# Optimization experiments

Hardware: AMD Instinct MI355X
Metric: run time of the kernel (lower is better)

Reference implementation:

```python
import jax, jax.numpy as jnp
import numpy as np

B, NELEC, NATOMS, SH_PER_ATOM, NORB, NCTR = 512, 100, 20, 30, 300, 2
NBAS = NATOMS * SH_PER_ATOM  # 600 == NORB * NCTR


def _ipow(x, k):
    # x**k for integer k in {0,1,2}; safe for negative x (cartesian harmonics)
    return jnp.where(k == 0, jnp.ones_like(x), jnp.where(k == 1, x, x * x))


def setup_inputs() -> dict:
    key = jax.random.key(0)
    ks = jax.random.split(key, 7)
    pos = jax.random.normal(ks[0], (B, NELEC * 3), jnp.float32)
    atom_coords = jax.random.normal(ks[1], (NATOMS, 3), jnp.float32)
    bas_exp = jax.random.uniform(ks[2], (NBAS,), jnp.float32, 0.5, 3.0)
    bas_n = jax.random.randint(ks[3], (NBAS,), 0, 3).astype(jnp.float32)
    norm_cst = jax.random.uniform(ks[4], (NBAS,), jnp.float32, 0.5, 1.5)
    bas_coeffs = jax.random.normal(ks[5], (NBAS,), jnp.float32)
    bas_kxyz = jax.random.randint(ks[6], (NBAS, 3), 0, 3)  # kx, ky, kz exponents
    index_ctr = jnp.repeat(jnp.arange(NORB, dtype=jnp.int32), NCTR)  # nbas -> norb
    return {"pos": pos, "atom_coords": atom_coords, "bas_exp": bas_exp,
            "bas_n": bas_n, "norm_cst": norm_cst, "bas_coeffs": bas_coeffs,
            "bas_kxyz": bas_kxyz, "index_ctr": index_ctr}


def reference(pos, atom_coords, bas_exp, bas_n, norm_cst, bas_coeffs, bas_kxyz, index_ctr):
    # gather: per-shell atom coordinates  (NBAS, 3)
    bas_coords = jnp.repeat(atom_coords, SH_PER_ATOM, axis=0)
    # electron - basis-center displacement  (B, Nelec, NBAS, 3)
    xyz = pos.reshape(-1, NELEC, 1, 3) - bas_coords[None, None]
    r2 = jnp.sum(xyz * xyz, axis=-1)                 # (B, Nelec, NBAS)
    r = jnp.sqrt(r2)
    # radial_gaussian: r^n * exp(-alpha r^2)
    R = jnp.power(r, bas_n) * jnp.exp(-bas_exp * r2)
    # cartesian harmonics: x^kx * y^ky * z^kz
    Y = (_ipow(xyz[..., 0], bas_kxyz[:, 0]) *
         _ipow(xyz[..., 1], bas_kxyz[:, 1]) *
         _ipow(xyz[..., 2], bas_kxyz[:, 2]))
    # ao kernel + contraction (segment-sum over basis fns into orbitals)
    vals = (norm_cst * bas_coeffs) * R * Y           # (B, Nelec, NBAS)
    ao = jnp.zeros((pos.shape[0], NELEC, NORB), vals.dtype).at[:, :, index_ctr].add(vals)
    return ao
```

## Files before the change

### kernel.cpp

```cpp
#include <hip/hip_runtime.h>

#define BATCH   512
#define NELEC   100
#define NATOMS  20
#define SH      30
#define NORB    300
#define NBAS    600
#define NROWS   (BATCH * NELEC)
#define ROWS    32
#define NBLOCKS (NROWS / ROWS)
#define BLOCK   320

#define LOG2E 1.4426950408889634f

__global__ __launch_bounds__(BLOCK, 8) void ao_kernel(
    const float* __restrict__ pos,
    const float* __restrict__ atom_coords,
    const float* __restrict__ bas_exp,
    const float* __restrict__ bas_n,
    const float* __restrict__ norm_cst,
    const float* __restrict__ bas_coeffs,
    const int*   __restrict__ bas_kxyz,
    float*       __restrict__ out)
{
    __shared__ float4 spos4[ROWS];

    const int t    = threadIdx.x;
    const int row0 = blockIdx.x * ROWS;

    if (t < ROWS * 3) {
        ((float*)spos4)[(t / 3) * 4 + (t % 3)] = pos[(size_t)row0 * 3 + t];
    }
    __syncthreads();

    if (t < NORB) {
        const int s0 = 2 * t, s1 = s0 + 1;

        const float al0 = bas_exp[s0] * LOG2E;
        const float al1 = bas_exp[s1] * LOG2E;
        const int   n0  = (int)bas_n[s0];
        const int   n1  = (int)bas_n[s1];
        const float c0  = norm_cst[s0] * bas_coeffs[s0];
        const float c1  = norm_cst[s1] * bas_coeffs[s1];
        const int  kx0 = bas_kxyz[3 * s0 + 0], ky0 = bas_kxyz[3 * s0 + 1], kz0 = bas_kxyz[3 * s0 + 2];
        const int  kx1 = bas_kxyz[3 * s1 + 0], ky1 = bas_kxyz[3 * s1 + 1], kz1 = bas_kxyz[3 * s1 + 2];
        const int  at  = s0 / SH;
        const float ax = atom_coords[3 * at + 0];
        const float ay = atom_coords[3 * at + 1];
        const float az = atom_coords[3 * at + 2];

        float* op = out + (size_t)row0 * NORB + t;

#pragma unroll 2
        for (int r = 0; r < ROWS; ++r) {
            const float4 p = spos4[r];

            const float dx = p.x - ax, dy = p.y - ay, dz = p.z - az;
            const float r2 = fmaf(dx, dx, fmaf(dy, dy, dz * dz));
            const float rr = sqrtf(r2);

            float e0 = exp2f(-al0 * r2);
            float R0 = (n0 == 0) ? 1.0f : ((n0 == 1) ? rr : r2);
            float yx = (kx0 == 0) ? 1.0f : dx;  yx = (kx0 == 2) ? yx * dx : yx;
            float yy = (ky0 == 0) ? 1.0f : dy;  yy = (ky0 == 2) ? yy * dy : yy;
            float yz = (kz0 == 0) ? 1.0f : dz;  yz = (kz0 == 2) ? yz * dz : yz;
            float v  = c0 * R0 * e0 * (yx * yy * yz);

            float e1 = exp2f(-al1 * r2);
            float R1 = (n1 == 0) ? 1.0f : ((n1 == 1) ? rr : r2);
            yx = (kx1 == 0) ? 1.0f : dx;  yx = (kx1 == 2) ? yx * dx : yx;
            yy = (ky1 == 0) ? 1.0f : dy;  yy = (ky1 == 2) ? yy * dy : yy;
            yz = (kz1 == 0) ? 1.0f : dz;  yz = (kz1 == 2) ? yz * dz : yz;
            v += c1 * R1 * e1 * (yx * yy * yz);

            *op = v;
            op += NORB;
        }
    }
}

extern "C" void kernel_launch(void* const* d_in, const int* in_sizes, int n_in,
                              void* d_out, int out_size, void* d_ws, size_t ws_size,
                              hipStream_t stream) {
    const float* pos         = (const float*)d_in[0];
    const float* atom_coords = (const float*)d_in[1];
    const float* bas_exp     = (const float*)d_in[2];
    const float* bas_n       = (const float*)d_in[3];
    const float* norm_cst    = (const float*)d_in[4];
    const float* bas_coeffs  = (const float*)d_in[5];
    const int*   bas_kxyz    = (const int*)d_in[6];
    float* out = (float*)d_out;

    ao_kernel<<<NBLOCKS, BLOCK, 0, stream>>>(pos, atom_coords, bas_exp, bas_n,
                                             norm_cst, bas_coeffs, bas_kxyz, out);
}
```

Measured before the change: 115.7 us.

## Vectorize basis-pair math with packed FMA and raw exp2/sqrt intrinsics

Replaces the per-basis selects with polynomial masks evaluated through packed two-wide FMAs, so both contracted basis functions are computed with packed-math instructions. It uses raw hardware exp2 and sqrt intrinsics, loads the per-thread parameters as vector loads before the barrier, and halves rows per block to launch more blocks. The raw intrinsics skip denormal and range handling, and smaller blocks repeat the parameter setup more often.

```diff
diff --git a/kernel.cpp b/kernel.cpp
--- a/kernel.cpp
+++ b/kernel.cpp
@@ -7,11 +7,16 @@
 #define NORB    300
 #define NBAS    600
 #define NROWS   (BATCH * NELEC)
-#define ROWS    32
-#define NBLOCKS (NROWS / ROWS)
+#define GROWS   16
+#define NBLOCKS (NROWS / GROWS)
 #define BLOCK   320
 
 #define LOG2E 1.4426950408889634f
+
+typedef float f2 __attribute__((ext_vector_type(2)));
+__device__ __forceinline__ f2 fma2(f2 a, f2 b, f2 c) {
+    return __builtin_elementwise_fma(a, b, c);
+}
 
 __global__ __launch_bounds__(BLOCK, 8) void ao_kernel(
     const float* __restrict__ pos,
@@ -23,57 +28,78 @@
     const int*   __restrict__ bas_kxyz,
     float*       __restrict__ out)
 {
-    __shared__ float4 spos4[ROWS];
+    __shared__ float4 spos4[GROWS];
 
     const int t    = threadIdx.x;
-    const int row0 = blockIdx.x * ROWS;
+    const int row0 = blockIdx.x * GROWS;
 
-    if (t < ROWS * 3) {
+    float2 ex2, nn2, nc2, bc2;
+    int2 k01, k23, k45;
+    float ax = 0.f, ay = 0.f, az = 0.f;
+    if (t < NORB) {
+        ex2 = ((const float2*)bas_exp)[t];
+        nn2 = ((const float2*)bas_n)[t];
+        nc2 = ((const float2*)norm_cst)[t];
+        bc2 = ((const float2*)bas_coeffs)[t];
+        k01 = ((const int2*)bas_kxyz)[3 * t + 0];
+        k23 = ((const int2*)bas_kxyz)[3 * t + 1];
+        k45 = ((const int2*)bas_kxyz)[3 * t + 2];
+        const int at = (2 * t) / SH;
+        ax = atom_coords[3 * at + 0];
+        ay = atom_coords[3 * at + 1];
+        az = atom_coords[3 * at + 2];
+    }
+
+    if (t < GROWS * 3) {
         ((float*)spos4)[(t / 3) * 4 + (t % 3)] = pos[(size_t)row0 * 3 + t];
     }
     __syncthreads();
 
     if (t < NORB) {
-        const int s0 = 2 * t, s1 = s0 + 1;
-
-        const float al0 = bas_exp[s0] * LOG2E;
-        const float al1 = bas_exp[s1] * LOG2E;
-        const int   n0  = (int)bas_n[s0];
-        const int   n1  = (int)bas_n[s1];
-        const float c0  = norm_cst[s0] * bas_coeffs[s0];
-        const float c1  = norm_cst[s1] * bas_coeffs[s1];
-        const int  kx0 = bas_kxyz[3 * s0 + 0], ky0 = bas_kxyz[3 * s0 + 1], kz0 = bas_kxyz[3 * s0 + 2];
-        const int  kx1 = bas_kxyz[3 * s1 + 0], ky1 = bas_kxyz[3 * s1 + 1], kz1 = bas_kxyz[3 * s1 + 2];
-        const int  at  = s0 / SH;
-        const float ax = atom_coords[3 * at + 0];
-        const float ay = atom_coords[3 * at + 1];
-        const float az = atom_coords[3 * at + 2];
+        const float c0 = nc2.x * bc2.x;
+        const float c1 = nc2.y * bc2.y;
+        const f2 al = { -ex2.x * LOG2E, -ex2.y * LOG2E };
+        const int n0 = (int)nn2.x, n1 = (int)nn2.y;
+        const f2 q0 = { (n0 == 0) ? c0 : 0.f, (n1 == 0) ? c1 : 0.f };
+        const f2 q1 = { (n0 == 1) ? c0 : 0.f, (n1 == 1) ? c1 : 0.f };
+        const f2 q2 = { (n0 == 2) ? c0 : 0.f, (n1 == 2) ? c1 : 0.f };
+        const int kx0 = k01.x, ky0 = k01.y, kz0 = k23.x;
+        const int kx1 = k23.y, ky1 = k45.x, kz1 = k45.y;
+        const f2 mx0 = { (float)(kx0 == 0), (float)(kx1 == 0) };
+        const f2 mx1 = { (float)(kx0 == 1), (float)(kx1 == 1) };
+        const f2 mx2 = { (float)(kx0 == 2), (float)(kx1 == 2) };
+        const f2 my0 = { (float)(ky0 == 0), (float)(ky1 == 0) };
+        const f2 my1 = { (float)(ky0 == 1), (float)(ky1 == 1) };
+        const f2 my2 = { (float)(ky0 == 2), (float)(ky1 == 2) };
+        const f2 mz0 = { (float)(kz0 == 0), (float)(kz1 == 0) };
+        const f2 mz1 = { (float)(kz0 == 1), (float)(kz1 == 1) };
+        const f2 mz2 = { (float)(kz0 == 2), (float)(kz1 == 2) };
 
         float* op = out + (size_t)row0 * NORB + t;
 
-#pragma unroll 2
-        for (int r = 0; r < ROWS; ++r) {
+#pragma unroll 4
+        for (int r = 0; r < GROWS; ++r) {
             const float4 p = spos4[r];
 
             const float dx = p.x - ax, dy = p.y - ay, dz = p.z - az;
-            const float r2 = fmaf(dx, dx, fmaf(dy, dy, dz * dz));
-            const float rr = sqrtf(r2);
+            const float r2s = fmaf(dx, dx, fmaf(dy, dy, dz * dz));
+            const float rr  = __builtin_amdgcn_sqrtf(r2s);
 
-            float e0 = exp2f(-al0 * r2);
-            float R0 = (n0 == 0) ? 1.0f : ((n0 == 1) ? rr : r2);
-            float yx = (kx0 == 0) ? 1.0f : dx;  yx = (kx0 == 2) ? yx * dx : yx;
-            float yy = (ky0 == 0) ? 1.0f : dy;  yy = (ky0 == 2) ? yy * dy : yy;
-            float yz = (kz0 == 0) ? 1.0f : dz;  yz = (kz0 == 2) ? yz * dz : yz;
-            float v  = c0 * R0 * e0 * (yx * yy * yz);
+            const f2 dxv = { dx, dx }, dyv = { dy, dy }, dzv = { dz, dz };
+            const f2 r2v = { r2s, r2s }, rrv = { rr, rr };
 
-            float e1 = exp2f(-al1 * r2);
-            float R1 = (n1 == 0) ? 1.0f : ((n1 == 1) ? rr : r2);
-            yx = (kx1 == 0) ? 1.0f : dx;  yx = (kx1 == 2) ? yx * dx : yx;
-            yy = (ky1 == 0) ? 1.0f : dy;  yy = (ky1 == 2) ? yy * dy : yy;
-            yz = (kz1 == 0) ? 1.0f : dz;  yz = (kz1 == 2) ? yz * dz : yz;
-            v += c1 * R1 * e1 * (yx * yy * yz);
+            const f2 ta = al * r2v;
+            f2 e;
+            e.x = __builtin_amdgcn_exp2f(ta.x);
+            e.y = __builtin_amdgcn_exp2f(ta.y);
 
-            *op = v;
+            const f2 cR = fma2(rrv, q1, fma2(r2v, q2, q0));
+            const f2 yx = fma2(dxv, fma2(dxv, mx2, mx1), mx0);
+            const f2 yy = fma2(dyv, fma2(dyv, my2, my1), my0);
+            const f2 yz = fma2(dzv, fma2(dzv, mz2, mz1), mz0);
+
+            const f2 w = (cR * e) * ((yx * yy) * yz);
+            *op = w.x + w.y;
             op += NORB;
         }
     }
```

New measurement: 100.8 us. -12.9%, faster.
